# Performance work log

Hardware: AMD Instinct MI355X
Metric: run time of the kernel (lower is better)

Reference implementation:

```python
import jax, jax.numpy as jnp
import numpy as np

SEGMENT_LENGTHS = [1024, 2048, 4096]
DILATION_RATES = [1, 2, 4]


def _head_groups(num_heads, num_segments):
    base = num_heads // num_segments
    extra = num_heads % num_segments
    groups = [base] * num_segments
    for i in range(extra):
        groups[-(i + 1)] += 1
    return groups


def _dilated_indices(segment_len, dilation_rate, offset):
    # Mirrors RingDilatedAttentionV2._apply_dilation index construction (static).
    if dilation_rate > 1:
        idx = np.arange(offset, segment_len, dilation_rate)
        repeats = (segment_len + len(idx) - 1) // len(idx)
        idx = np.tile(idx, repeats)[:segment_len] % segment_len
    else:
        idx = np.arange(segment_len)
    return jnp.asarray(idx, dtype=jnp.int32)


def setup_inputs() -> dict:
    key = jax.random.key(0)
    kq, kk, kv = jax.random.split(key, 3)
    b, n, h, d = 1, 4096, 12, 64
    return {
        "query": jax.random.normal(kq, (b, n, h, d), dtype=jnp.float32),
        "key": jax.random.normal(kk, (b, n, h, d), dtype=jnp.float32),
        "value": jax.random.normal(kv, (b, n, h, d), dtype=jnp.float32),
        "is_causal": 1,
    }


def _dilated_attention(query, key, value, is_causal):
    b, n, h, d = query.shape
    groups = _head_groups(h, len(SEGMENT_LENGTHS))
    scale = 1.0 / np.sqrt(d).astype(np.float32)
    outs = []
    head_start = 0
    for i, (seg_len, rate, g) in enumerate(zip(SEGMENT_LENGTHS, DILATION_RATES, groups)):
        if g == 0:
            continue
        sl = min(seg_len, n)
        ns = n // sl  # n chosen divisible by every segment length
        q = query[:, :, head_start:head_start + g, :].reshape(b, ns, sl, g, d)
        k = key[:, :, head_start:head_start + g, :].reshape(b, ns, sl, g, d)
        v = value[:, :, head_start:head_start + g, :].reshape(b, ns, sl, g, d)
        if rate > 1 or i > 0:
            idx = _dilated_indices(sl, rate, i)
            k = k[:, :, idx]
            v = v[:, :, idx]
        # scores: [b, seg, heads, q_pos, k_pos]
        scores = jnp.einsum("bsqhd,bskhd->bshqk", q, k) * scale
        if is_causal:
            causal = jnp.triu(jnp.ones((sl, sl), dtype=bool), k=1)
            scores = jnp.where(causal, jnp.finfo(scores.dtype).min, scores)
        attn = jax.nn.softmax(scores, axis=-1)
        o = jnp.einsum("bshqk,bskhd->bsqhd", attn, v).reshape(b, n, g, d)
        outs.append(o)
        head_start += g
    return jnp.concatenate(outs, axis=2)  # [b, n, h, d]


def reference(query, key, value, is_causal):
    return _dilated_attention(query, key, value, is_causal)
```

## Files before the change

kernel.cpp:

```cpp
#include <hip/hip_runtime.h>
#include <hip/hip_bf16.h>
#include <math.h>

typedef __bf16 bf16x8 __attribute__((ext_vector_type(8)));
typedef float  f32x4  __attribute__((ext_vector_type(4)));
typedef float  f32x16 __attribute__((ext_vector_type(16)));
typedef int    int2v  __attribute__((ext_vector_type(2)));
typedef unsigned int uint4v __attribute__((ext_vector_type(4)));
typedef unsigned short ushort_t;

#define LDK 72

#define KG_OFF  0
#define VGT_OFF 6291456
#define LACC_OFF 12582912
#define CTR_OFF  12779520

struct ItemTab { unsigned short v[896]; int n; };

constexpr ItemTab build_items(int causal) {
    ItemTab t{};
    for (int i = 0; i < 896; ++i) t.v[i] = 0xFFFF;
    t.n = 0;
    for (int cost = 16; cost >= 1; --cost)
        for (int qt = 31; qt >= 0; --qt)
            for (int h = 11; h >= 0; --h) {
                const int group = h >> 2;
                const int sl = 1024 << group;
                const int qb = (qt << 7) & (sl - 1);
                const int nkt = causal ? (((qb + 127) >> 6) + 1) : (sl >> 6);
                for (int c = 0; c < 4; ++c) {
                    const int kt0 = c << 4;
                    if (kt0 >= nkt) continue;
                    const int rem = nkt - kt0;
                    const int cst = rem < 16 ? rem : 16;
                    if (cst == cost) t.v[t.n++] = (unsigned short)((qt << 6) | (h << 2) | c);
                }
            }
    return t;
}

__constant__ ItemTab g_tab_c = build_items(1);
__constant__ ItemTab g_tab_n = build_items(0);

__device__ __forceinline__ int gather_pos(int gi, int group) {
    const int lsl = 10 + group;
    const int seg = gi >> lsl;
    const int j   = gi - (seg << lsl);
    return (seg << lsl) + group + ((j & 1023) << group);
}

__device__ __forceinline__ void gld_lds16(const ushort_t* g, __bf16* l) {
    __builtin_amdgcn_global_load_lds(
        (const __attribute__((address_space(1))) void*)g,
        (__attribute__((address_space(3))) void*)l, 16, 0, 0);
}

__device__ __forceinline__ unsigned int pk_bf16(float lo, float hi) {
    unsigned short a = __builtin_bit_cast(unsigned short, (__bf16)lo);
    unsigned short b = __builtin_bit_cast(unsigned short, (__bf16)hi);
    return ((unsigned int)b << 16) | (unsigned int)a;
}

__device__ __forceinline__ f32x16 zero16() {
    f32x16 z;
    #pragma unroll
    for (int i = 0; i < 16; ++i) z[i] = 0.f;
    return z;
}

__global__ __launch_bounds__(256)
void preconvert_kernel(const float* __restrict__ K, const float* __restrict__ V,
                       ushort_t* __restrict__ Kg, ushort_t* __restrict__ VgT,
                       float* __restrict__ Out, float* __restrict__ l_acc,
                       int* __restrict__ ctr)
{
    const int HD = 768;
    int b = blockIdx.x;
    const int tid = threadIdx.x;
    if (b < 768) {
        if (b == 0 && tid == 0) *ctr = 0;
        {
            float4 z = {0.f, 0.f, 0.f, 0.f};
            float4* zp = (float4*)Out + ((size_t)b * 256 + tid) * 4;
            zp[0] = z; zp[1] = z; zp[2] = z; zp[3] = z;
        }
        const int h = b % 12, gi0 = (b / 12) * 64;
        const int group = h >> 2;
        const int gi = gi0 + (tid >> 2);
        const int d0 = (tid & 3) << 4;
        const int pos = gather_pos(gi, group);
        const float* kp = K + (size_t)pos * HD + h * 64 + d0;
        float4 x0 = ((const float4*)kp)[0], x1 = ((const float4*)kp)[1];
        float4 x2 = ((const float4*)kp)[2], x3 = ((const float4*)kp)[3];
        bf16x8 w0, w1;
        w0[0]=(__bf16)x0.x; w0[1]=(__bf16)x0.y; w0[2]=(__bf16)x0.z; w0[3]=(__bf16)x0.w;
        w0[4]=(__bf16)x1.x; w0[5]=(__bf16)x1.y; w0[6]=(__bf16)x1.z; w0[7]=(__bf16)x1.w;
        w1[0]=(__bf16)x2.x; w1[1]=(__bf16)x2.y; w1[2]=(__bf16)x2.z; w1[3]=(__bf16)x2.w;
        w1[4]=(__bf16)x3.x; w1[5]=(__bf16)x3.y; w1[6]=(__bf16)x3.z; w1[7]=(__bf16)x3.w;
        ushort_t* out = Kg + ((size_t)(h * 4096 + gi)) * 64 + d0;
        *(bf16x8*)out = w0;
        *(bf16x8*)(out + 8) = w1;
    } else {
        b -= 768;
        if (b < 192) l_acc[b * 256 + tid] = 0.f;
        const int h = b % 12, gi0 = (b / 12) * 64;
        const int group = h >> 2;
        __shared__ __align__(16) __bf16 Ts[64 * LDK];
        const int gil = tid >> 2;
        const int d0 = (tid & 3) << 4;
        const int pos = gather_pos(gi0 + gil, group);
        const float* vp = V + (size_t)pos * HD + h * 64 + d0;
        float4 x0 = ((const float4*)vp)[0], x1 = ((const float4*)vp)[1];
        float4 x2 = ((const float4*)vp)[2], x3 = ((const float4*)vp)[3];
        bf16x8 w0, w1;
        w0[0]=(__bf16)x0.x; w0[1]=(__bf16)x0.y; w0[2]=(__bf16)x0.z; w0[3]=(__bf16)x0.w;
        w0[4]=(__bf16)x1.x; w0[5]=(__bf16)x1.y; w0[6]=(__bf16)x1.z; w0[7]=(__bf16)x1.w;
        w1[0]=(__bf16)x2.x; w1[1]=(__bf16)x2.y; w1[2]=(__bf16)x2.z; w1[3]=(__bf16)x2.w;
        w1[4]=(__bf16)x3.x; w1[5]=(__bf16)x3.y; w1[6]=(__bf16)x3.z; w1[7]=(__bf16)x3.w;
        *(bf16x8*)&Ts[gil * LDK + d0]     = w0;
        *(bf16x8*)&Ts[gil * LDK + d0 + 8] = w1;
        __syncthreads();
        const int d = tid >> 2, c = tid & 3;
        bf16x8 o0, o1;
        #pragma unroll
        for (int i = 0; i < 8; ++i) {
            o0[i] = Ts[(c * 16 + i) * LDK + d];
            o1[i] = Ts[(c * 16 + 8 + i) * LDK + d];
        }
        ushort_t* out = VgT + ((size_t)(h * 64 + d)) * 4096 + gi0 + c * 16;
        *(bf16x8*)out = o0;
        *(bf16x8*)(out + 8) = o1;
    }
}

__global__ __launch_bounds__(256)
void dilated_attn_kernel(const float* __restrict__ Q,
                         const ushort_t* __restrict__ Kg,
                         const ushort_t* __restrict__ VgT,
                         const int* __restrict__ is_causal_p,
                         float* __restrict__ Out,
                         float* __restrict__ l_acc,
                         int* __restrict__ ctr)
{
    const int HD = 768;
    const int causal = (*is_causal_p) != 0;
    const ItemTab& tab = causal ? g_tab_c : g_tab_n;
    const int n_items = tab.n;

    const int tid  = threadIdx.x;
    const int wave = tid >> 6;
    const int lane = tid & 63;
    const int l31  = lane & 31;
    const int hi   = lane >> 5;

    __shared__ __align__(16) __bf16 Ks[2][64 * 64];
    __shared__ __align__(16) __bf16 Vs[2][64 * 64];
    __shared__ int s_item;

    const int bx16 = (((lane & 7) ^ (lane >> 3)) & 7) << 3;
    const int r8   = lane >> 3;

    for (;;) {
        if (tid == 0) s_item = atomicAdd(ctr, 1);
        __syncthreads();
        const int n = s_item;
        __syncthreads();
        if (n >= n_items) break;

        const int enc = tab.v[n];
        const int qt  = enc >> 6;
        const int h   = (enc >> 2) & 15;
        const int c   = enc & 3;
        const int group = h >> 2;
        const int sl    = 1024 << group;

        const int q0 = qt << 7;
        const int qb = q0 & (sl - 1);
        const int seg_start = q0 - qb;
        const int blk_diag = (qb + 127) >> 6;
        const int nkt = causal ? (blk_diag + 1) : (sl >> 6);
        const int kt0 = c << 4;
        const int kend = min(kt0 + 16, nkt);
        const int nch  = (nkt + 15) >> 4;

        const ushort_t* kg_head = Kg + (size_t)h * 4096 * 64;
        const ushort_t* vt_head = VgT + (size_t)h * 64 * 4096;

        auto stage = [&](int kt, int buf) {
            const ushort_t* kb = kg_head + ((size_t)(seg_start + (kt << 6)) << 6);
            const ushort_t* vb = vt_head + seg_start + (kt << 6);
            #pragma unroll
            for (int i = 0; i < 2; ++i) {
                const int row = i * 32 + wave * 8 + r8;
                gld_lds16(kb + row * 64 + bx16, &Ks[buf][(i * 32 + wave * 8) * 64]);
                gld_lds16(vb + (size_t)row * 4096 + bx16, &Vs[buf][(i * 32 + wave * 8) * 64]);
            }
        };

        stage(kt0, 0);

        const int qrow = q0 + wave * 32 + l31;
        const float* qptr = Q + (size_t)qrow * HD + h * 64;
        bf16x8 qf[4];
        {
            const float s = 0.125f * 1.4426950408889634f;
            #pragma unroll
            for (int ds = 0; ds < 4; ++ds) {
                float4 x0 = ((const float4*)(qptr + ds * 16 + hi * 8))[0];
                float4 x1 = ((const float4*)(qptr + ds * 16 + hi * 8))[1];
                bf16x8 w;
                w[0]=(__bf16)(x0.x*s); w[1]=(__bf16)(x0.y*s); w[2]=(__bf16)(x0.z*s); w[3]=(__bf16)(x0.w*s);
                w[4]=(__bf16)(x1.x*s); w[5]=(__bf16)(x1.y*s); w[6]=(__bf16)(x1.z*s); w[7]=(__bf16)(x1.w*s);
                qf[ds] = w;
            }
        }

        const int mydiag = causal ? ((qb + wave * 32 + 31) >> 6) : 0x7fffffff;
        const int lrow   = ((wave & 1) << 5) + l31;

        f32x16 o0 = zero16(), o1 = zero16();
        float l_part = 0.f;

        for (int kt = kt0; kt < kend; ++kt) {
            const int cur = (kt - kt0) & 1;

            asm volatile("s_waitcnt vmcnt(0)" ::: "memory");
            __builtin_amdgcn_s_barrier();
            __builtin_amdgcn_sched_barrier(0);

            if (kt + 1 < kend) stage(kt + 1, cur ^ 1);

            if (kt <= mydiag) {
                f32x16 s0 = zero16(), s1 = zero16();
                const int xr = (l31 & 7);
                __builtin_amdgcn_s_setprio(1);
                #pragma unroll
                for (int ds = 0; ds < 4; ++ds) {
                    const int cb = ds * 2 + hi;
                    bf16x8 k0 = *(const bf16x8*)&Ks[cur][l31 * 64        + ((cb ^ xr) << 3)];
                    bf16x8 k1 = *(const bf16x8*)&Ks[cur][(32 + l31) * 64 + ((cb ^ xr) << 3)];
                    s0 = __builtin_amdgcn_mfma_f32_32x32x16_bf16(k0, qf[ds], s0, 0, 0, 0);
                    s1 = __builtin_amdgcn_mfma_f32_32x32x16_bf16(k1, qf[ds], s1, 0, 0, 0);
                }
                __builtin_amdgcn_s_setprio(0);

                float p[2][16];
                const bool isdiag = causal && (kt == mydiag);
                #pragma unroll
                for (int r = 0; r < 16; ++r) {
                    float v0 = __builtin_amdgcn_exp2f(s0[r]);
                    float v1 = __builtin_amdgcn_exp2f(s1[r]);
                    if (isdiag) {
                        const int kl = (r & 3) + ((r >> 2) << 3) + (hi << 2);
                        if (kl > lrow)      v0 = 0.f;
                        if (kl + 32 > lrow) v1 = 0.f;
                    }
                    p[0][r] = v0; p[1][r] = v1;
                    l_part += v0 + v1;
                }

                __builtin_amdgcn_s_setprio(1);
                #pragma unroll
                for (int b = 0; b < 2; ++b) {
                    #pragma unroll
                    for (int ks2 = 0; ks2 < 2; ++ks2) {
                        const int g = ks2 * 8;
                        int x0 = (int)pk_bf16(p[b][g + 0], p[b][g + 1]);
                        int x1 = (int)pk_bf16(p[b][g + 2], p[b][g + 3]);
                        int y0 = (int)pk_bf16(p[b][g + 4], p[b][g + 5]);
                        int y1 = (int)pk_bf16(p[b][g + 6], p[b][g + 7]);
                        int2v r02 = __builtin_amdgcn_permlane32_swap(x0, y0, false, false);
                        int2v r13 = __builtin_amdgcn_permlane32_swap(x1, y1, false, false);
                        uint4v t;
                        t[0] = (unsigned int)r02[0];
                        t[1] = (unsigned int)r13[0];
                        t[2] = (unsigned int)r02[1];
                        t[3] = (unsigned int)r13[1];
                        bf16x8 pa = __builtin_bit_cast(bf16x8, t);
                        const int kcb = (b * 2 + ks2) * 2 + hi;
                        bf16x8 v0 = *(const bf16x8*)&Vs[cur][l31 * 64        + ((kcb ^ xr) << 3)];
                        bf16x8 v1 = *(const bf16x8*)&Vs[cur][(32 + l31) * 64 + ((kcb ^ xr) << 3)];
                        o0 = __builtin_amdgcn_mfma_f32_32x32x16_bf16(pa, v0, o0, 0, 0, 0);
                        o1 = __builtin_amdgcn_mfma_f32_32x32x16_bf16(pa, v1, o1, 0, 0, 0);
                    }
                }
                __builtin_amdgcn_s_setprio(0);
            }
        }

        const float l2 = l_part + __shfl_xor(l_part, 32);
        const int qw = q0 + wave * 32;
        if (nch == 1) {
            const float inv = 1.0f / l2;
            #pragma unroll
            for (int r = 0; r < 16; ++r) {
                const int qloc = (r & 3) + ((r >> 2) << 3) + (hi << 2);
                const float invq = __shfl(inv, qloc);
                const int row = qw + qloc;
                Out[(size_t)row * HD + h * 64 + l31]      = o0[r] * invq;
                Out[(size_t)row * HD + h * 64 + 32 + l31] = o1[r] * invq;
            }
        } else {
            if (hi == 0) atomicAdd(&l_acc[(qw + l31) * 12 + h], l2);
            #pragma unroll
            for (int r = 0; r < 16; ++r) {
                const int qloc = (r & 3) + ((r >> 2) << 3) + (hi << 2);
                const int row = qw + qloc;
                atomicAdd(&Out[(size_t)row * HD + h * 64 + l31],      o0[r]);
                atomicAdd(&Out[(size_t)row * HD + h * 64 + 32 + l31], o1[r]);
            }
        }
    }
}

__global__ __launch_bounds__(256)
void finalize_kernel(float* __restrict__ Out, const float* __restrict__ l_acc,
                     const int* __restrict__ is_causal_p)
{
    const int causal = (*is_causal_p) != 0;
    const int idx = blockIdx.x * 256 + threadIdx.x;
    const int rh = idx >> 4;
    const int d4 = idx & 15;
    const int h = rh % 12;
    const int row = rh / 12;
    const int group = h >> 2;
    const int ntf = 16 << group;
    const int qt128 = row >> 7;
    const int qb_t = (qt128 << 1) & (ntf - 1);
    const int nkt = causal ? (qb_t + 2) : ntf;
    if (nkt <= 16) return;
    const float inv = 1.0f / l_acc[rh];
    float4* p = (float4*)Out + (size_t)rh * 16 + d4;
    float4 v = *p;
    v.x *= inv; v.y *= inv; v.z *= inv; v.w *= inv;
    *p = v;
}

extern "C" void kernel_launch(void* const* d_in, const int* in_sizes, int n_in,
                              void* d_out, int out_size, void* d_ws, size_t ws_size,
                              hipStream_t stream) {
    (void)in_sizes; (void)n_in; (void)out_size; (void)ws_size;
    const float* Q = (const float*)d_in[0];
    const float* K = (const float*)d_in[1];
    const float* V = (const float*)d_in[2];
    const int* isc = (const int*)d_in[3];
    float* Out = (float*)d_out;
    ushort_t* Kg   = (ushort_t*)((char*)d_ws + KG_OFF);
    ushort_t* VgT  = (ushort_t*)((char*)d_ws + VGT_OFF);
    float*    lacc = (float*)((char*)d_ws + LACC_OFF);
    int*      ctr  = (int*)((char*)d_ws + CTR_OFF);

    preconvert_kernel<<<1536, 256, 0, stream>>>(K, V, Kg, VgT, Out, lacc, ctr);
    dilated_attn_kernel<<<512, 256, 0, stream>>>(Q, Kg, VgT, isc, Out, lacc, ctr);
    finalize_kernel<<<3072, 256, 0, stream>>>(Out, lacc, isc);
}
```

Measured before the change: 135.2 us.

## Fuse preconvert, attention and finalize into one cooperative kernel with grid syncs

Merges the three launches into a single cooperative kernel of 512 blocks that runs grid-stride preconvert units, then the attention work queue, then finalize, separated by grid.sync. Preconvert K is rewritten to read each source row once and write it to all its dilated gather slots. Zeroing of Out is limited to rows that take multi-chunk atomics. The aim is to remove launch gaps and redundant global traffic, at the cost of grid-wide barriers and higher LDS use per block, which could cut occupancy. A fallback to the three-kernel path is kept in case the cooperative launch fails.

```diff
diff --git a/kernel.cpp b/kernel.cpp
--- a/kernel.cpp
+++ b/kernel.cpp
@@ -1,6 +1,9 @@
 #include <hip/hip_runtime.h>
 #include <hip/hip_bf16.h>
+#include <hip/hip_cooperative_groups.h>
 #include <math.h>
+
+namespace cg = cooperative_groups;
 
 typedef __bf16 bf16x8 __attribute__((ext_vector_type(8)));
 typedef float  f32x4  __attribute__((ext_vector_type(4)));
@@ -69,44 +72,60 @@
     return z;
 }
 
-__global__ __launch_bounds__(256)
-void preconvert_kernel(const float* __restrict__ K, const float* __restrict__ V,
-                       ushort_t* __restrict__ Kg, ushort_t* __restrict__ VgT,
-                       float* __restrict__ Out, float* __restrict__ l_acc,
-                       int* __restrict__ ctr)
+__device__ __forceinline__ void preconvert_unit(
+    int b, int tid, const float* __restrict__ K, const float* __restrict__ V,
+    ushort_t* __restrict__ Kg, ushort_t* __restrict__ VgT,
+    float* __restrict__ Out, float* __restrict__ l_acc,
+    int* __restrict__ ctr, int causal, __bf16* Ts)
 {
     const int HD = 768;
-    int b = blockIdx.x;
-    const int tid = threadIdx.x;
     if (b < 768) {
         if (b == 0 && tid == 0) *ctr = 0;
         {
-            float4 z = {0.f, 0.f, 0.f, 0.f};
-            float4* zp = (float4*)Out + ((size_t)b * 256 + tid) * 4;
-            zp[0] = z; zp[1] = z; zp[2] = z; zp[3] = z;
-        }
-        const int h = b % 12, gi0 = (b / 12) * 64;
+            const int rh = (b * 256 + tid) >> 2;
+            const int h_ = rh % 12;
+            const int row_ = rh / 12;
+            const int ntf = 16 << (h_ >> 2);
+            const int qt128 = row_ >> 7;
+            const int qb_t = (qt128 << 1) & (ntf - 1);
+            const int nkt = causal ? (qb_t + 2) : ntf;
+            if (nkt > 16) {
+                float4 z = {0.f, 0.f, 0.f, 0.f};
+                float4* zp = (float4*)Out + ((size_t)b * 256 + tid) * 4;
+                zp[0] = z; zp[1] = z; zp[2] = z; zp[3] = z;
+            }
+        }
+        const int h = b % 12, p0 = (b / 12) * 64;
         const int group = h >> 2;
-        const int gi = gi0 + (tid >> 2);
+        const int pos = p0 + (tid >> 2);
         const int d0 = (tid & 3) << 4;
-        const int pos = gather_pos(gi, group);
-        const float* kp = K + (size_t)pos * HD + h * 64 + d0;
-        float4 x0 = ((const float4*)kp)[0], x1 = ((const float4*)kp)[1];
-        float4 x2 = ((const float4*)kp)[2], x3 = ((const float4*)kp)[3];
-        bf16x8 w0, w1;
-        w0[0]=(__bf16)x0.x; w0[1]=(__bf16)x0.y; w0[2]=(__bf16)x0.z; w0[3]=(__bf16)x0.w;
-        w0[4]=(__bf16)x1.x; w0[5]=(__bf16)x1.y; w0[6]=(__bf16)x1.z; w0[7]=(__bf16)x1.w;
-        w1[0]=(__bf16)x2.x; w1[1]=(__bf16)x2.y; w1[2]=(__bf16)x2.z; w1[3]=(__bf16)x2.w;
-        w1[4]=(__bf16)x3.x; w1[5]=(__bf16)x3.y; w1[6]=(__bf16)x3.z; w1[7]=(__bf16)x3.w;
-        ushort_t* out = Kg + ((size_t)(h * 4096 + gi)) * 64 + d0;
-        *(bf16x8*)out = w0;
-        *(bf16x8*)(out + 8) = w1;
+        const int lsl = 10 + group;
+        const int rate = 1 << group;
+        const int seg_base = (pos >> lsl) << lsl;
+        const int po = pos - seg_base;
+        const int rem = po - group;
+        if (rem >= 0 && (rem & (rate - 1)) == 0) {
+            const float* kp = K + (size_t)pos * HD + h * 64 + d0;
+            float4 x0 = ((const float4*)kp)[0], x1 = ((const float4*)kp)[1];
+            float4 x2 = ((const float4*)kp)[2], x3 = ((const float4*)kp)[3];
+            bf16x8 w0, w1;
+            w0[0]=(__bf16)x0.x; w0[1]=(__bf16)x0.y; w0[2]=(__bf16)x0.z; w0[3]=(__bf16)x0.w;
+            w0[4]=(__bf16)x1.x; w0[5]=(__bf16)x1.y; w0[6]=(__bf16)x1.z; w0[7]=(__bf16)x1.w;
+            w1[0]=(__bf16)x2.x; w1[1]=(__bf16)x2.y; w1[2]=(__bf16)x2.z; w1[3]=(__bf16)x2.w;
+            w1[4]=(__bf16)x3.x; w1[5]=(__bf16)x3.y; w1[6]=(__bf16)x3.z; w1[7]=(__bf16)x3.w;
+            const int jb = rem >> group;
+            for (int k = 0; k < rate; ++k) {
+                const int gi = seg_base + jb + (k << 10);
+                ushort_t* out = Kg + ((size_t)(h * 4096 + gi)) * 64 + d0;
+                *(bf16x8*)out = w0;
+                *(bf16x8*)(out + 8) = w1;
+            }
+        }
     } else {
         b -= 768;
         if (b < 192) l_acc[b * 256 + tid] = 0.f;
         const int h = b % 12, gi0 = (b / 12) * 64;
         const int group = h >> 2;
-        __shared__ __align__(16) __bf16 Ts[64 * LDK];
         const int gil = tid >> 2;
         const int d0 = (tid & 3) << 4;
         const int pos = gather_pos(gi0 + gil, group);
@@ -131,20 +150,17 @@
         ushort_t* out = VgT + ((size_t)(h * 64 + d)) * 4096 + gi0 + c * 16;
         *(bf16x8*)out = o0;
         *(bf16x8*)(out + 8) = o1;
+        __syncthreads();
     }
 }
 
-__global__ __launch_bounds__(256)
-void dilated_attn_kernel(const float* __restrict__ Q,
-                         const ushort_t* __restrict__ Kg,
-                         const ushort_t* __restrict__ VgT,
-                         const int* __restrict__ is_causal_p,
-                         float* __restrict__ Out,
-                         float* __restrict__ l_acc,
-                         int* __restrict__ ctr)
+__device__ __forceinline__ void attn_phase(
+    const float* __restrict__ Q, const ushort_t* __restrict__ Kg,
+    const ushort_t* __restrict__ VgT, int causal,
+    float* __restrict__ Out, float* __restrict__ l_acc, int* __restrict__ ctr,
+    __bf16 (*Ks)[64 * 64], __bf16 (*Vs)[64 * 64], int* s_item)
 {
     const int HD = 768;
-    const int causal = (*is_causal_p) != 0;
     const ItemTab& tab = causal ? g_tab_c : g_tab_n;
     const int n_items = tab.n;
 
@@ -154,17 +170,13 @@
     const int l31  = lane & 31;
     const int hi   = lane >> 5;
 
-    __shared__ __align__(16) __bf16 Ks[2][64 * 64];
-    __shared__ __align__(16) __bf16 Vs[2][64 * 64];
-    __shared__ int s_item;
-
     const int bx16 = (((lane & 7) ^ (lane >> 3)) & 7) << 3;
     const int r8   = lane >> 3;
 
     for (;;) {
-        if (tid == 0) s_item = atomicAdd(ctr, 1);
+        if (tid == 0) *s_item = atomicAdd(ctr, 1);
         __syncthreads();
-        const int n = s_item;
+        const int n = *s_item;
         __syncthreads();
         if (n >= n_items) break;
 
@@ -261,6 +273,7 @@
                 }
 
                 __builtin_amdgcn_s_setprio(1);
+                const int xr2 = (l31 & 7);
                 #pragma unroll
                 for (int b = 0; b < 2; ++b) {
                     #pragma unroll
@@ -279,8 +292,8 @@
                         t[3] = (unsigned int)r13[1];
                         bf16x8 pa = __builtin_bit_cast(bf16x8, t);
                         const int kcb = (b * 2 + ks2) * 2 + hi;
-                        bf16x8 v0 = *(const bf16x8*)&Vs[cur][l31 * 64        + ((kcb ^ xr) << 3)];
-                        bf16x8 v1 = *(const bf16x8*)&Vs[cur][(32 + l31) * 64 + ((kcb ^ xr) << 3)];
+                        bf16x8 v0 = *(const bf16x8*)&Vs[cur][l31 * 64        + ((kcb ^ xr2) << 3)];
+                        bf16x8 v1 = *(const bf16x8*)&Vs[cur][(32 + l31) * 64 + ((kcb ^ xr2) << 3)];
                         o0 = __builtin_amdgcn_mfma_f32_32x32x16_bf16(pa, v0, o0, 0, 0, 0);
                         o1 = __builtin_amdgcn_mfma_f32_32x32x16_bf16(pa, v1, o1, 0, 0, 0);
                     }
@@ -314,18 +327,14 @@
     }
 }
 
-__global__ __launch_bounds__(256)
-void finalize_kernel(float* __restrict__ Out, const float* __restrict__ l_acc,
-                     const int* __restrict__ is_causal_p)
-{
-    const int causal = (*is_causal_p) != 0;
-    const int idx = blockIdx.x * 256 + threadIdx.x;
+__device__ __forceinline__ void finalize_unit(
+    int idx, float* __restrict__ Out, const float* __restrict__ l_acc, int causal)
+{
     const int rh = idx >> 4;
     const int d4 = idx & 15;
     const int h = rh % 12;
     const int row = rh / 12;
-    const int group = h >> 2;
-    const int ntf = 16 << group;
+    const int ntf = 16 << (h >> 2);
     const int qt128 = row >> 7;
     const int qb_t = (qt128 << 1) & (ntf - 1);
     const int nkt = causal ? (qb_t + 2) : ntf;
@@ -335,6 +344,68 @@
     float4 v = *p;
     v.x *= inv; v.y *= inv; v.z *= inv; v.w *= inv;
     *p = v;
+}
+
+__global__ __launch_bounds__(256)
+void fused_kernel(const float* __restrict__ Q, const float* __restrict__ K,
+                  const float* __restrict__ V, const int* __restrict__ is_causal_p,
+                  float* __restrict__ Out, ushort_t* __restrict__ Kg,
+                  ushort_t* __restrict__ VgT, float* __restrict__ l_acc,
+                  int* __restrict__ ctr)
+{
+    __shared__ __align__(16) __bf16 Ks[2][64 * 64];
+    __shared__ __align__(16) __bf16 Vs[2][64 * 64];
+    __shared__ __align__(16) __bf16 Ts[64 * LDK];
+    __shared__ int s_item;
+
+    cg::grid_group grid = cg::this_grid();
+    const int causal = (*is_causal_p) != 0;
+    const int tid = threadIdx.x;
+
+    for (int u = blockIdx.x; u < 1536; u += 512)
+        preconvert_unit(u, tid, K, V, Kg, VgT, Out, l_acc, ctr, causal, Ts);
+
+    grid.sync();
+
+    attn_phase(Q, Kg, VgT, causal, Out, l_acc, ctr, Ks, Vs, &s_item);
+
+    grid.sync();
+
+    for (int base = blockIdx.x; base < 3072; base += 512)
+        finalize_unit(base * 256 + tid, Out, l_acc, causal);
+}
+
+__global__ __launch_bounds__(256)
+void preconvert_kernel(const float* __restrict__ K, const float* __restrict__ V,
+                       ushort_t* __restrict__ Kg, ushort_t* __restrict__ VgT,
+                       float* __restrict__ Out, float* __restrict__ l_acc,
+                       int* __restrict__ ctr, const int* __restrict__ is_causal_p)
+{
+    __shared__ __align__(16) __bf16 Ts[64 * LDK];
+    preconvert_unit(blockIdx.x, threadIdx.x, K, V, Kg, VgT, Out, l_acc, ctr,
+                    (*is_causal_p) != 0, Ts);
+}
+
+__global__ __launch_bounds__(256)
+void dilated_attn_kernel(const float* __restrict__ Q,
+                         const ushort_t* __restrict__ Kg,
+                         const ushort_t* __restrict__ VgT,
+                         const int* __restrict__ is_causal_p,
+                         float* __restrict__ Out,
+                         float* __restrict__ l_acc,
+                         int* __restrict__ ctr)
+{
+    __shared__ __align__(16) __bf16 Ks[2][64 * 64];
+    __shared__ __align__(16) __bf16 Vs[2][64 * 64];
+    __shared__ int s_item;
+    attn_phase(Q, Kg, VgT, (*is_causal_p) != 0, Out, l_acc, ctr, Ks, Vs, &s_item);
+}
+
+__global__ __launch_bounds__(256)
+void finalize_kernel(float* __restrict__ Out, const float* __restrict__ l_acc,
+                     const int* __restrict__ is_causal_p)
+{
+    finalize_unit(blockIdx.x * 256 + threadIdx.x, Out, l_acc, (*is_causal_p) != 0);
 }
 
 extern "C" void kernel_launch(void* const* d_in, const int* in_sizes, int n_in,
@@ -351,7 +422,14 @@
     float*    lacc = (float*)((char*)d_ws + LACC_OFF);
     int*      ctr  = (int*)((char*)d_ws + CTR_OFF);
 
-    preconvert_kernel<<<1536, 256, 0, stream>>>(K, V, Kg, VgT, Out, lacc, ctr);
-    dilated_attn_kernel<<<512, 256, 0, stream>>>(Q, Kg, VgT, isc, Out, lacc, ctr);
-    finalize_kernel<<<3072, 256, 0, stream>>>(Out, lacc, isc);
-}
+    void* args[] = {(void*)&Q, (void*)&K, (void*)&V, (void*)&isc, (void*)&Out,
+                    (void*)&Kg, (void*)&VgT, (void*)&lacc, (void*)&ctr};
+    hipError_t e = hipLaunchCooperativeKernel((const void*)fused_kernel,
+                                              dim3(512), dim3(256), args, 0, stream);
+    if (e != hipSuccess) {
+        (void)hipGetLastError();
+        preconvert_kernel<<<1536, 256, 0, stream>>>(K, V, Kg, VgT, Out, lacc, ctr, isc);
+        dilated_attn_kernel<<<512, 256, 0, stream>>>(Q, Kg, VgT, isc, Out, lacc, ctr);
+        finalize_kernel<<<3072, 256, 0, stream>>>(Out, lacc, isc);
+    }
+}
```

New measurement: 275.7 us. +103.9%, slower.

## Halve split-K chunk size, double persistent grid, dedupe K gather writes

Applied to the files above, without the earlier changes.

Work items now cover 8 key tiles instead of 16, which doubles the item count and gives finer load balancing. The persistent grid grows to 1024 blocks with a launch bound of 4 waves per SIMD. The K preconversion reads each source row once and writes it to every replicated gather slot. The output zeroing is skipped for rows that a single chunk writes directly. More items produce more atomic partial-sum adds into the output, and the V LDS swizzle index changes to use l31&7.

```diff
diff --git a/kernel.cpp b/kernel.cpp
--- a/kernel.cpp
+++ b/kernel.cpp
@@ -16,25 +16,25 @@
 #define LACC_OFF 12582912
 #define CTR_OFF  12779520
 
-struct ItemTab { unsigned short v[896]; int n; };
+struct ItemTab { unsigned short v[1792]; int n; };
 
 constexpr ItemTab build_items(int causal) {
     ItemTab t{};
-    for (int i = 0; i < 896; ++i) t.v[i] = 0xFFFF;
+    for (int i = 0; i < 1792; ++i) t.v[i] = 0xFFFF;
     t.n = 0;
-    for (int cost = 16; cost >= 1; --cost)
+    for (int cost = 8; cost >= 1; --cost)
         for (int qt = 31; qt >= 0; --qt)
             for (int h = 11; h >= 0; --h) {
                 const int group = h >> 2;
                 const int sl = 1024 << group;
                 const int qb = (qt << 7) & (sl - 1);
                 const int nkt = causal ? (((qb + 127) >> 6) + 1) : (sl >> 6);
-                for (int c = 0; c < 4; ++c) {
-                    const int kt0 = c << 4;
+                for (int c = 0; c < 8; ++c) {
+                    const int kt0 = c << 3;
                     if (kt0 >= nkt) continue;
                     const int rem = nkt - kt0;
-                    const int cst = rem < 16 ? rem : 16;
-                    if (cst == cost) t.v[t.n++] = (unsigned short)((qt << 6) | (h << 2) | c);
+                    const int cst = rem < 8 ? rem : 8;
+                    if (cst == cost) t.v[t.n++] = (unsigned short)((qt << 7) | (h << 3) | c);
                 }
             }
     return t;
@@ -73,7 +73,7 @@
 void preconvert_kernel(const float* __restrict__ K, const float* __restrict__ V,
                        ushort_t* __restrict__ Kg, ushort_t* __restrict__ VgT,
                        float* __restrict__ Out, float* __restrict__ l_acc,
-                       int* __restrict__ ctr)
+                       int* __restrict__ ctr, const int* __restrict__ is_causal_p)
 {
     const int HD = 768;
     int b = blockIdx.x;
@@ -81,26 +81,46 @@
     if (b < 768) {
         if (b == 0 && tid == 0) *ctr = 0;
         {
-            float4 z = {0.f, 0.f, 0.f, 0.f};
-            float4* zp = (float4*)Out + ((size_t)b * 256 + tid) * 4;
-            zp[0] = z; zp[1] = z; zp[2] = z; zp[3] = z;
-        }
-        const int h = b % 12, gi0 = (b / 12) * 64;
+            const int causal = (*is_causal_p) != 0;
+            const int rh = (b * 256 + tid) >> 2;
+            const int h_ = rh % 12;
+            const int row_ = rh / 12;
+            const int ntf = 16 << (h_ >> 2);
+            const int qt128 = row_ >> 7;
+            const int qb_t = (qt128 << 1) & (ntf - 1);
+            const int nkt = causal ? (qb_t + 2) : ntf;
+            if (nkt > 8) {
+                float4 z = {0.f, 0.f, 0.f, 0.f};
+                float4* zp = (float4*)Out + ((size_t)b * 256 + tid) * 4;
+                zp[0] = z; zp[1] = z; zp[2] = z; zp[3] = z;
+            }
+        }
+        const int h = b % 12, p0 = (b / 12) * 64;
         const int group = h >> 2;
-        const int gi = gi0 + (tid >> 2);
+        const int pos = p0 + (tid >> 2);
         const int d0 = (tid & 3) << 4;
-        const int pos = gather_pos(gi, group);
-        const float* kp = K + (size_t)pos * HD + h * 64 + d0;
-        float4 x0 = ((const float4*)kp)[0], x1 = ((const float4*)kp)[1];
-        float4 x2 = ((const float4*)kp)[2], x3 = ((const float4*)kp)[3];
-        bf16x8 w0, w1;
-        w0[0]=(__bf16)x0.x; w0[1]=(__bf16)x0.y; w0[2]=(__bf16)x0.z; w0[3]=(__bf16)x0.w;
-        w0[4]=(__bf16)x1.x; w0[5]=(__bf16)x1.y; w0[6]=(__bf16)x1.z; w0[7]=(__bf16)x1.w;
-        w1[0]=(__bf16)x2.x; w1[1]=(__bf16)x2.y; w1[2]=(__bf16)x2.z; w1[3]=(__bf16)x2.w;
-        w1[4]=(__bf16)x3.x; w1[5]=(__bf16)x3.y; w1[6]=(__bf16)x3.z; w1[7]=(__bf16)x3.w;
-        ushort_t* out = Kg + ((size_t)(h * 4096 + gi)) * 64 + d0;
-        *(bf16x8*)out = w0;
-        *(bf16x8*)(out + 8) = w1;
+        const int lsl = 10 + group;
+        const int rate = 1 << group;
+        const int seg_base = (pos >> lsl) << lsl;
+        const int po = pos - seg_base;
+        const int rem = po - group;
+        if (rem >= 0 && (rem & (rate - 1)) == 0) {
+            const float* kp = K + (size_t)pos * HD + h * 64 + d0;
+            float4 x0 = ((const float4*)kp)[0], x1 = ((const float4*)kp)[1];
+            float4 x2 = ((const float4*)kp)[2], x3 = ((const float4*)kp)[3];
+            bf16x8 w0, w1;
+            w0[0]=(__bf16)x0.x; w0[1]=(__bf16)x0.y; w0[2]=(__bf16)x0.z; w0[3]=(__bf16)x0.w;
+            w0[4]=(__bf16)x1.x; w0[5]=(__bf16)x1.y; w0[6]=(__bf16)x1.z; w0[7]=(__bf16)x1.w;
+            w1[0]=(__bf16)x2.x; w1[1]=(__bf16)x2.y; w1[2]=(__bf16)x2.z; w1[3]=(__bf16)x2.w;
+            w1[4]=(__bf16)x3.x; w1[5]=(__bf16)x3.y; w1[6]=(__bf16)x3.z; w1[7]=(__bf16)x3.w;
+            const int jb = rem >> group;
+            for (int k = 0; k < rate; ++k) {
+                const int gi = seg_base + jb + (k << 10);
+                ushort_t* out = Kg + ((size_t)(h * 4096 + gi)) * 64 + d0;
+                *(bf16x8*)out = w0;
+                *(bf16x8*)(out + 8) = w1;
+            }
+        }
     } else {
         b -= 768;
         if (b < 192) l_acc[b * 256 + tid] = 0.f;
@@ -134,7 +154,7 @@
     }
 }
 
-__global__ __launch_bounds__(256)
+__global__ __launch_bounds__(256, 4)
 void dilated_attn_kernel(const float* __restrict__ Q,
                          const ushort_t* __restrict__ Kg,
                          const ushort_t* __restrict__ VgT,
@@ -169,9 +189,9 @@
         if (n >= n_items) break;
 
         const int enc = tab.v[n];
-        const int qt  = enc >> 6;
-        const int h   = (enc >> 2) & 15;
-        const int c   = enc & 3;
+        const int qt  = enc >> 7;
+        const int h   = (enc >> 3) & 15;
+        const int c   = enc & 7;
         const int group = h >> 2;
         const int sl    = 1024 << group;
 
@@ -180,9 +200,9 @@
         const int seg_start = q0 - qb;
         const int blk_diag = (qb + 127) >> 6;
         const int nkt = causal ? (blk_diag + 1) : (sl >> 6);
-        const int kt0 = c << 4;
-        const int kend = min(kt0 + 16, nkt);
-        const int nch  = (nkt + 15) >> 4;
+        const int kt0 = c << 3;
+        const int kend = min(kt0 + 8, nkt);
+        const int nch  = (nkt + 7) >> 3;
 
         const ushort_t* kg_head = Kg + (size_t)h * 4096 * 64;
         const ushort_t* vt_head = VgT + (size_t)h * 64 * 4096;
@@ -261,6 +281,7 @@
                 }
 
                 __builtin_amdgcn_s_setprio(1);
+                const int xr2 = (l31 & 7);
                 #pragma unroll
                 for (int b = 0; b < 2; ++b) {
                     #pragma unroll
@@ -279,8 +300,8 @@
                         t[3] = (unsigned int)r13[1];
                         bf16x8 pa = __builtin_bit_cast(bf16x8, t);
                         const int kcb = (b * 2 + ks2) * 2 + hi;
-                        bf16x8 v0 = *(const bf16x8*)&Vs[cur][l31 * 64        + ((kcb ^ xr) << 3)];
-                        bf16x8 v1 = *(const bf16x8*)&Vs[cur][(32 + l31) * 64 + ((kcb ^ xr) << 3)];
+                        bf16x8 v0 = *(const bf16x8*)&Vs[cur][l31 * 64        + ((kcb ^ xr2) << 3)];
+                        bf16x8 v1 = *(const bf16x8*)&Vs[cur][(32 + l31) * 64 + ((kcb ^ xr2) << 3)];
                         o0 = __builtin_amdgcn_mfma_f32_32x32x16_bf16(pa, v0, o0, 0, 0, 0);
                         o1 = __builtin_amdgcn_mfma_f32_32x32x16_bf16(pa, v1, o1, 0, 0, 0);
                     }
@@ -324,12 +345,11 @@
     const int d4 = idx & 15;
     const int h = rh % 12;
     const int row = rh / 12;
-    const int group = h >> 2;
-    const int ntf = 16 << group;
+    const int ntf = 16 << (h >> 2);
     const int qt128 = row >> 7;
     const int qb_t = (qt128 << 1) & (ntf - 1);
     const int nkt = causal ? (qb_t + 2) : ntf;
-    if (nkt <= 16) return;
+    if (nkt <= 8) return;
     const float inv = 1.0f / l_acc[rh];
     float4* p = (float4*)Out + (size_t)rh * 16 + d4;
     float4 v = *p;
@@ -351,7 +371,7 @@
     float*    lacc = (float*)((char*)d_ws + LACC_OFF);
     int*      ctr  = (int*)((char*)d_ws + CTR_OFF);
 
-    preconvert_kernel<<<1536, 256, 0, stream>>>(K, V, Kg, VgT, Out, lacc, ctr);
-    dilated_attn_kernel<<<512, 256, 0, stream>>>(Q, Kg, VgT, isc, Out, lacc, ctr);
+    preconvert_kernel<<<1536, 256, 0, stream>>>(K, V, Kg, VgT, Out, lacc, ctr, isc);
+    dilated_attn_kernel<<<1024, 256, 0, stream>>>(Q, Kg, VgT, isc, Out, lacc, ctr);
     finalize_kernel<<<3072, 256, 0, stream>>>(Out, lacc, isc);
 }
```

Result: slower. 150.6 us (+11.4%).

## Partition attention work into per-XCD bins with XCC-local queues and dedupe K gather

Applied to the files above, without the earlier changes.

Splits the global work-item queue into 8 bins keyed by head, one atomic counter per bin. Each workgroup reads its XCC id and drains its own bin first, then moves round-robin to the others, so K/V tiles for a head tend to stay in one XCD's L2. The K preconvert now reads each source row once and writes it to every duplicated gather slot instead of gathering per output. Output zeroing is limited to rows that use atomic accumulation. The risks are load imbalance between bins, dependence on the XCC id register, and the added per-row predicate checks.

```diff
diff --git a/kernel.cpp b/kernel.cpp
--- a/kernel.cpp
+++ b/kernel.cpp
@@ -16,27 +16,33 @@
 #define LACC_OFF 12582912
 #define CTR_OFF  12779520
 
-struct ItemTab { unsigned short v[896]; int n; };
+struct ItemTab { unsigned short v[896]; int beg[9]; };
 
 constexpr ItemTab build_items(int causal) {
     ItemTab t{};
     for (int i = 0; i < 896; ++i) t.v[i] = 0xFFFF;
-    t.n = 0;
-    for (int cost = 16; cost >= 1; --cost)
-        for (int qt = 31; qt >= 0; --qt)
-            for (int h = 11; h >= 0; --h) {
-                const int group = h >> 2;
-                const int sl = 1024 << group;
-                const int qb = (qt << 7) & (sl - 1);
-                const int nkt = causal ? (((qb + 127) >> 6) + 1) : (sl >> 6);
-                for (int c = 0; c < 4; ++c) {
-                    const int kt0 = c << 4;
-                    if (kt0 >= nkt) continue;
-                    const int rem = nkt - kt0;
-                    const int cst = rem < 16 ? rem : 16;
-                    if (cst == cost) t.v[t.n++] = (unsigned short)((qt << 6) | (h << 2) | c);
-                }
-            }
+    const int head2bin[12] = {4, 5, 6, 7, 4, 5, 6, 7, 0, 1, 2, 3};
+    int n = 0;
+    for (int bin = 0; bin < 8; ++bin) {
+        t.beg[bin] = n;
+        for (int cost = 16; cost >= 1; --cost)
+            for (int qt = 31; qt >= 0; --qt)
+                for (int h = 11; h >= 0; --h) {
+                    if (head2bin[h] != bin) continue;
+                    const int group = h >> 2;
+                    const int sl = 1024 << group;
+                    const int qb = (qt << 7) & (sl - 1);
+                    const int nkt = causal ? (((qb + 127) >> 6) + 1) : (sl >> 6);
+                    for (int c = 0; c < 4; ++c) {
+                        const int kt0 = c << 4;
+                        if (kt0 >= nkt) continue;
+                        const int rem = nkt - kt0;
+                        const int cst = rem < 16 ? rem : 16;
+                        if (cst == cost) t.v[n++] = (unsigned short)((qt << 6) | (h << 2) | c);
+                    }
+                }
+    }
+    t.beg[8] = n;
     return t;
 }
 
@@ -73,34 +79,54 @@
 void preconvert_kernel(const float* __restrict__ K, const float* __restrict__ V,
                        ushort_t* __restrict__ Kg, ushort_t* __restrict__ VgT,
                        float* __restrict__ Out, float* __restrict__ l_acc,
-                       int* __restrict__ ctr)
+                       int* __restrict__ ctr, const int* __restrict__ is_causal_p)
 {
     const int HD = 768;
     int b = blockIdx.x;
     const int tid = threadIdx.x;
     if (b < 768) {
-        if (b == 0 && tid == 0) *ctr = 0;
+        if (b == 0 && tid < 8) ctr[tid] = 0;
         {
-            float4 z = {0.f, 0.f, 0.f, 0.f};
-            float4* zp = (float4*)Out + ((size_t)b * 256 + tid) * 4;
-            zp[0] = z; zp[1] = z; zp[2] = z; zp[3] = z;
+            const int causal = (*is_causal_p) != 0;
+            const int rh = (b * 256 + tid) >> 2;
+            const int h_ = rh % 12;
+            const int row_ = rh / 12;
+            const int ntf = 16 << (h_ >> 2);
+            const int qt128 = row_ >> 7;
+            const int qb_t = (qt128 << 1) & (ntf - 1);
+            const int nkt = causal ? (qb_t + 2) : ntf;
+            if (nkt > 16) {
+                float4 z = {0.f, 0.f, 0.f, 0.f};
+                float4* zp = (float4*)Out + ((size_t)b * 256 + tid) * 4;
+                zp[0] = z; zp[1] = z; zp[2] = z; zp[3] = z;
+            }
         }
-        const int h = b % 12, gi0 = (b / 12) * 64;
+        const int h = b % 12, p0 = (b / 12) * 64;
         const int group = h >> 2;
-        const int gi = gi0 + (tid >> 2);
+        const int pos = p0 + (tid >> 2);
         const int d0 = (tid & 3) << 4;
-        const int pos = gather_pos(gi, group);
-        const float* kp = K + (size_t)pos * HD + h * 64 + d0;
-        float4 x0 = ((const float4*)kp)[0], x1 = ((const float4*)kp)[1];
-        float4 x2 = ((const float4*)kp)[2], x3 = ((const float4*)kp)[3];
-        bf16x8 w0, w1;
-        w0[0]=(__bf16)x0.x; w0[1]=(__bf16)x0.y; w0[2]=(__bf16)x0.z; w0[3]=(__bf16)x0.w;
-        w0[4]=(__bf16)x1.x; w0[5]=(__bf16)x1.y; w0[6]=(__bf16)x1.z; w0[7]=(__bf16)x1.w;
-        w1[0]=(__bf16)x2.x; w1[1]=(__bf16)x2.y; w1[2]=(__bf16)x2.z; w1[3]=(__bf16)x2.w;
-        w1[4]=(__bf16)x3.x; w1[5]=(__bf16)x3.y; w1[6]=(__bf16)x3.z; w1[7]=(__bf16)x3.w;
-        ushort_t* out = Kg + ((size_t)(h * 4096 + gi)) * 64 + d0;
-        *(bf16x8*)out = w0;
-        *(bf16x8*)(out + 8) = w1;
+        const int lsl = 10 + group;
+        const int rate = 1 << group;
+        const int seg_base = (pos >> lsl) << lsl;
+        const int po = pos - seg_base;
+        const int rem = po - group;
+        if (rem >= 0 && (rem & (rate - 1)) == 0) {
+            const float* kp = K + (size_t)pos * HD + h * 64 + d0;
+            float4 x0 = ((const float4*)kp)[0], x1 = ((const float4*)kp)[1];
+            float4 x2 = ((const float4*)kp)[2], x3 = ((const float4*)kp)[3];
+            bf16x8 w0, w1;
+            w0[0]=(__bf16)x0.x; w0[1]=(__bf16)x0.y; w0[2]=(__bf16)x0.z; w0[3]=(__bf16)x0.w;
+            w0[4]=(__bf16)x1.x; w0[5]=(__bf16)x1.y; w0[6]=(__bf16)x1.z; w0[7]=(__bf16)x1.w;
+            w1[0]=(__bf16)x2.x; w1[1]=(__bf16)x2.y; w1[2]=(__bf16)x2.z; w1[3]=(__bf16)x2.w;
+            w1[4]=(__bf16)x3.x; w1[5]=(__bf16)x3.y; w1[6]=(__bf16)x3.z; w1[7]=(__bf16)x3.w;
+            const int jb = rem >> group;
+            for (int k = 0; k < rate; ++k) {
+                const int gi = seg_base + jb + (k << 10);
+                ushort_t* out = Kg + ((size_t)(h * 4096 + gi)) * 64 + d0;
+                *(bf16x8*)out = w0;
+                *(bf16x8*)(out + 8) = w1;
+            }
+        }
     } else {
         b -= 768;
         if (b < 192) l_acc[b * 256 + tid] = 0.f;
@@ -146,7 +172,6 @@
     const int HD = 768;
     const int causal = (*is_causal_p) != 0;
     const ItemTab& tab = causal ? g_tab_c : g_tab_n;
-    const int n_items = tab.n;
 
     const int tid  = threadIdx.x;
     const int wave = tid >> 6;
@@ -158,157 +183,165 @@
     __shared__ __align__(16) __bf16 Vs[2][64 * 64];
     __shared__ int s_item;
 
+    unsigned int xcc = 0;
+    asm volatile("s_getreg_b32 %0, hwreg(HW_REG_XCC_ID)" : "=s"(xcc));
+    const int myx = (int)(xcc & 7);
+
     const int bx16 = (((lane & 7) ^ (lane >> 3)) & 7) << 3;
     const int r8   = lane >> 3;
 
-    for (;;) {
-        if (tid == 0) s_item = atomicAdd(ctr, 1);
-        __syncthreads();
-        const int n = s_item;
-        __syncthreads();
-        if (n >= n_items) break;
-
-        const int enc = tab.v[n];
-        const int qt  = enc >> 6;
-        const int h   = (enc >> 2) & 15;
-        const int c   = enc & 3;
-        const int group = h >> 2;
-        const int sl    = 1024 << group;
-
-        const int q0 = qt << 7;
-        const int qb = q0 & (sl - 1);
-        const int seg_start = q0 - qb;
-        const int blk_diag = (qb + 127) >> 6;
-        const int nkt = causal ? (blk_diag + 1) : (sl >> 6);
-        const int kt0 = c << 4;
-        const int kend = min(kt0 + 16, nkt);
-        const int nch  = (nkt + 15) >> 4;
-
-        const ushort_t* kg_head = Kg + (size_t)h * 4096 * 64;
-        const ushort_t* vt_head = VgT + (size_t)h * 64 * 4096;
-
-        auto stage = [&](int kt, int buf) {
-            const ushort_t* kb = kg_head + ((size_t)(seg_start + (kt << 6)) << 6);
-            const ushort_t* vb = vt_head + seg_start + (kt << 6);
-            #pragma unroll
-            for (int i = 0; i < 2; ++i) {
-                const int row = i * 32 + wave * 8 + r8;
-                gld_lds16(kb + row * 64 + bx16, &Ks[buf][(i * 32 + wave * 8) * 64]);
-                gld_lds16(vb + (size_t)row * 4096 + bx16, &Vs[buf][(i * 32 + wave * 8) * 64]);
-            }
-        };
-
-        stage(kt0, 0);
-
-        const int qrow = q0 + wave * 32 + l31;
-        const float* qptr = Q + (size_t)qrow * HD + h * 64;
-        bf16x8 qf[4];
-        {
-            const float s = 0.125f * 1.4426950408889634f;
-            #pragma unroll
-            for (int ds = 0; ds < 4; ++ds) {
-                float4 x0 = ((const float4*)(qptr + ds * 16 + hi * 8))[0];
-                float4 x1 = ((const float4*)(qptr + ds * 16 + hi * 8))[1];
-                bf16x8 w;
-                w[0]=(__bf16)(x0.x*s); w[1]=(__bf16)(x0.y*s); w[2]=(__bf16)(x0.z*s); w[3]=(__bf16)(x0.w*s);
-                w[4]=(__bf16)(x1.x*s); w[5]=(__bf16)(x1.y*s); w[6]=(__bf16)(x1.z*s); w[7]=(__bf16)(x1.w*s);
-                qf[ds] = w;
-            }
-        }
-
-        const int mydiag = causal ? ((qb + wave * 32 + 31) >> 6) : 0x7fffffff;
-        const int lrow   = ((wave & 1) << 5) + l31;
-
-        f32x16 o0 = zero16(), o1 = zero16();
-        float l_part = 0.f;
-
-        for (int kt = kt0; kt < kend; ++kt) {
-            const int cur = (kt - kt0) & 1;
-
-            asm volatile("s_waitcnt vmcnt(0)" ::: "memory");
-            __builtin_amdgcn_s_barrier();
-            __builtin_amdgcn_sched_barrier(0);
-
-            if (kt + 1 < kend) stage(kt + 1, cur ^ 1);
-
-            if (kt <= mydiag) {
-                f32x16 s0 = zero16(), s1 = zero16();
-                const int xr = (l31 & 7);
-                __builtin_amdgcn_s_setprio(1);
+    for (int ring = 0; ring < 8; ++ring) {
+        const int bin = (myx + ring) & 7;
+        const int lo = tab.beg[bin], hicap = tab.beg[bin + 1];
+        for (;;) {
+            if (tid == 0) s_item = lo + atomicAdd(&ctr[bin], 1);
+            __syncthreads();
+            const int n = s_item;
+            __syncthreads();
+            if (n >= hicap) break;
+
+            const int enc = tab.v[n];
+            const int qt  = enc >> 6;
+            const int h   = (enc >> 2) & 15;
+            const int c   = enc & 3;
+            const int group = h >> 2;
+            const int sl    = 1024 << group;
+
+            const int q0 = qt << 7;
+            const int qb = q0 & (sl - 1);
+            const int seg_start = q0 - qb;
+            const int blk_diag = (qb + 127) >> 6;
+            const int nkt = causal ? (blk_diag + 1) : (sl >> 6);
+            const int kt0 = c << 4;
+            const int kend = min(kt0 + 16, nkt);
+            const int nch  = (nkt + 15) >> 4;
+
+            const ushort_t* kg_head = Kg + (size_t)h * 4096 * 64;
+            const ushort_t* vt_head = VgT + (size_t)h * 64 * 4096;
+
+            auto stage = [&](int kt, int buf) {
+                const ushort_t* kb = kg_head + ((size_t)(seg_start + (kt << 6)) << 6);
+                const ushort_t* vb = vt_head + seg_start + (kt << 6);
+                #pragma unroll
+                for (int i = 0; i < 2; ++i) {
+                    const int row = i * 32 + wave * 8 + r8;
+                    gld_lds16(kb + row * 64 + bx16, &Ks[buf][(i * 32 + wave * 8) * 64]);
+                    gld_lds16(vb + (size_t)row * 4096 + bx16, &Vs[buf][(i * 32 + wave * 8) * 64]);
+                }
+            };
+
+            stage(kt0, 0);
+
+            const int qrow = q0 + wave * 32 + l31;
+            const float* qptr = Q + (size_t)qrow * HD + h * 64;
+            bf16x8 qf[4];
+            {
+                const float s = 0.125f * 1.4426950408889634f;
                 #pragma unroll
                 for (int ds = 0; ds < 4; ++ds) {
-                    const int cb = ds * 2 + hi;
-                    bf16x8 k0 = *(const bf16x8*)&Ks[cur][l31 * 64        + ((cb ^ xr) << 3)];
-                    bf16x8 k1 = *(const bf16x8*)&Ks[cur][(32 + l31) * 64 + ((cb ^ xr) << 3)];
-                    s0 = __builtin_amdgcn_mfma_f32_32x32x16_bf16(k0, qf[ds], s0, 0, 0, 0);
-                    s1 = __builtin_amdgcn_mfma_f32_32x32x16_bf16(k1, qf[ds], s1, 0, 0, 0);
-                }
-                __builtin_amdgcn_s_setprio(0);
-
-                float p[2][16];
-                const bool isdiag = causal && (kt == mydiag);
+                    float4 x0 = ((const float4*)(qptr + ds * 16 + hi * 8))[0];
+                    float4 x1 = ((const float4*)(qptr + ds * 16 + hi * 8))[1];
+                    bf16x8 w;
+                    w[0]=(__bf16)(x0.x*s); w[1]=(__bf16)(x0.y*s); w[2]=(__bf16)(x0.z*s); w[3]=(__bf16)(x0.w*s);
+                    w[4]=(__bf16)(x1.x*s); w[5]=(__bf16)(x1.y*s); w[6]=(__bf16)(x1.z*s); w[7]=(__bf16)(x1.w*s);
+                    qf[ds] = w;
+                }
+            }
+
+            const int mydiag = causal ? ((qb + wave * 32 + 31) >> 6) : 0x7fffffff;
+            const int lrow   = ((wave & 1) << 5) + l31;
+
+            f32x16 o0 = zero16(), o1 = zero16();
+            float l_part = 0.f;
+
+            for (int kt = kt0; kt < kend; ++kt) {
+                const int cur = (kt - kt0) & 1;
+
+                asm volatile("s_waitcnt vmcnt(0)" ::: "memory");
+                __builtin_amdgcn_s_barrier();
+                __builtin_amdgcn_sched_barrier(0);
+
+                if (kt + 1 < kend) stage(kt + 1, cur ^ 1);
+
+                if (kt <= mydiag) {
+                    f32x16 s0 = zero16(), s1 = zero16();
+                    const int xr = (l31 & 7);
+                    __builtin_amdgcn_s_setprio(1);
+                    #pragma unroll
+                    for (int ds = 0; ds < 4; ++ds) {
+                        const int cb = ds * 2 + hi;
+                        bf16x8 k0 = *(const bf16x8*)&Ks[cur][l31 * 64        + ((cb ^ xr) << 3)];
+                        bf16x8 k1 = *(const bf16x8*)&Ks[cur][(32 + l31) * 64 + ((cb ^ xr) << 3)];
+                        s0 = __builtin_amdgcn_mfma_f32_32x32x16_bf16(k0, qf[ds], s0, 0, 0, 0);
+                        s1 = __builtin_amdgcn_mfma_f32_32x32x16_bf16(k1, qf[ds], s1, 0, 0, 0);
+                    }
+                    __builtin_amdgcn_s_setprio(0);
+
+                    float p[2][16];
+                    const bool isdiag = causal && (kt == mydiag);
+                    #pragma unroll
+                    for (int r = 0; r < 16; ++r) {
+                        float v0 = __builtin_amdgcn_exp2f(s0[r]);
+                        float v1 = __builtin_amdgcn_exp2f(s1[r]);
+                        if (isdiag) {
+                            const int kl = (r & 3) + ((r >> 2) << 3) + (hi << 2);
+                            if (kl > lrow)      v0 = 0.f;
+                            if (kl + 32 > lrow) v1 = 0.f;
+                        }
+                        p[0][r] = v0; p[1][r] = v1;
+                        l_part += v0 + v1;
+                    }
+
+                    __builtin_amdgcn_s_setprio(1);
+                    #pragma unroll
+                    for (int b = 0; b < 2; ++b) {
+                        #pragma unroll
+                        for (int ks2 = 0; ks2 < 2; ++ks2) {
+                            const int g = ks2 * 8;
+                            int x0 = (int)pk_bf16(p[b][g + 0], p[b][g + 1]);
+                            int x1 = (int)pk_bf16(p[b][g + 2], p[b][g + 3]);
+                            int y0 = (int)pk_bf16(p[b][g + 4], p[b][g + 5]);
+                            int y1 = (int)pk_bf16(p[b][g + 6], p[b][g + 7]);
+                            int2v r02 = __builtin_amdgcn_permlane32_swap(x0, y0, false, false);
+                            int2v r13 = __builtin_amdgcn_permlane32_swap(x1, y1, false, false);
+                            uint4v t;
+                            t[0] = (unsigned int)r02[0];
+                            t[1] = (unsigned int)r13[0];
+                            t[2] = (unsigned int)r02[1];
+                            t[3] = (unsigned int)r13[1];
+                            bf16x8 pa = __builtin_bit_cast(bf16x8, t);
+                            const int kcb = (b * 2 + ks2) * 2 + hi;
+                            bf16x8 v0 = *(const bf16x8*)&Vs[cur][l31 * 64        + ((kcb ^ xr) << 3)];
+                            bf16x8 v1 = *(const bf16x8*)&Vs[cur][(32 + l31) * 64 + ((kcb ^ xr) << 3)];
+                            o0 = __builtin_amdgcn_mfma_f32_32x32x16_bf16(pa, v0, o0, 0, 0, 0);
+                            o1 = __builtin_amdgcn_mfma_f32_32x32x16_bf16(pa, v1, o1, 0, 0, 0);
+                        }
+                    }
+                    __builtin_amdgcn_s_setprio(0);
+                }
+            }
+
+            const float l2 = l_part + __shfl_xor(l_part, 32);
+            const int qw = q0 + wave * 32;
+            if (nch == 1) {
+                const float inv = 1.0f / l2;
                 #pragma unroll
                 for (int r = 0; r < 16; ++r) {
-                    float v0 = __builtin_amdgcn_exp2f(s0[r]);
-                    float v1 = __builtin_amdgcn_exp2f(s1[r]);
-                    if (isdiag) {
-                        const int kl = (r & 3) + ((r >> 2) << 3) + (hi << 2);
-                        if (kl > lrow)      v0 = 0.f;
-                        if (kl + 32 > lrow) v1 = 0.f;
-                    }
-                    p[0][r] = v0; p[1][r] = v1;
-                    l_part += v0 + v1;
-                }
-
-                __builtin_amdgcn_s_setprio(1);
+                    const int qloc = (r & 3) + ((r >> 2) << 3) + (hi << 2);
+                    const float invq = __shfl(inv, qloc);
+                    const int row = qw + qloc;
+                    Out[(size_t)row * HD + h * 64 + l31]      = o0[r] * invq;
+                    Out[(size_t)row * HD + h * 64 + 32 + l31] = o1[r] * invq;
+                }
+            } else {
+                if (hi == 0) atomicAdd(&l_acc[(qw + l31) * 12 + h], l2);
                 #pragma unroll
-                for (int b = 0; b < 2; ++b) {
-                    #pragma unroll
-                    for (int ks2 = 0; ks2 < 2; ++ks2) {
-                        const int g = ks2 * 8;
-                        int x0 = (int)pk_bf16(p[b][g + 0], p[b][g + 1]);
-                        int x1 = (int)pk_bf16(p[b][g + 2], p[b][g + 3]);
-                        int y0 = (int)pk_bf16(p[b][g + 4], p[b][g + 5]);
-                        int y1 = (int)pk_bf16(p[b][g + 6], p[b][g + 7]);
-                        int2v r02 = __builtin_amdgcn_permlane32_swap(x0, y0, false, false);
-                        int2v r13 = __builtin_amdgcn_permlane32_swap(x1, y1, false, false);
-                        uint4v t;
-                        t[0] = (unsigned int)r02[0];
-                        t[1] = (unsigned int)r13[0];
-                        t[2] = (unsigned int)r02[1];
-                        t[3] = (unsigned int)r13[1];
-                        bf16x8 pa = __builtin_bit_cast(bf16x8, t);
-                        const int kcb = (b * 2 + ks2) * 2 + hi;
-                        bf16x8 v0 = *(const bf16x8*)&Vs[cur][l31 * 64        + ((kcb ^ xr) << 3)];
-                        bf16x8 v1 = *(const bf16x8*)&Vs[cur][(32 + l31) * 64 + ((kcb ^ xr) << 3)];
-                        o0 = __builtin_amdgcn_mfma_f32_32x32x16_bf16(pa, v0, o0, 0, 0, 0);
-                        o1 = __builtin_amdgcn_mfma_f32_32x32x16_bf16(pa, v1, o1, 0, 0, 0);
-                    }
-                }
-                __builtin_amdgcn_s_setprio(0);
-            }
-        }
-
-        const float l2 = l_part + __shfl_xor(l_part, 32);
-        const int qw = q0 + wave * 32;
-        if (nch == 1) {
-            const float inv = 1.0f / l2;
-            #pragma unroll
-            for (int r = 0; r < 16; ++r) {
-                const int qloc = (r & 3) + ((r >> 2) << 3) + (hi << 2);
-                const float invq = __shfl(inv, qloc);
-                const int row = qw + qloc;
-                Out[(size_t)row * HD + h * 64 + l31]      = o0[r] * invq;
-                Out[(size_t)row * HD + h * 64 + 32 + l31] = o1[r] * invq;
-            }
-        } else {
-            if (hi == 0) atomicAdd(&l_acc[(qw + l31) * 12 + h], l2);
-            #pragma unroll
-            for (int r = 0; r < 16; ++r) {
-                const int qloc = (r & 3) + ((r >> 2) << 3) + (hi << 2);
-                const int row = qw + qloc;
-                atomicAdd(&Out[(size_t)row * HD + h * 64 + l31],      o0[r]);
-                atomicAdd(&Out[(size_t)row * HD + h * 64 + 32 + l31], o1[r]);
+                for (int r = 0; r < 16; ++r) {
+                    const int qloc = (r & 3) + ((r >> 2) << 3) + (hi << 2);
+                    const int row = qw + qloc;
+                    atomicAdd(&Out[(size_t)row * HD + h * 64 + l31],      o0[r]);
+                    atomicAdd(&Out[(size_t)row * HD + h * 64 + 32 + l31], o1[r]);
+                }
             }
         }
     }
@@ -324,8 +357,7 @@
     const int d4 = idx & 15;
     const int h = rh % 12;
     const int row = rh / 12;
-    const int group = h >> 2;
-    const int ntf = 16 << group;
+    const int ntf = 16 << (h >> 2);
     const int qt128 = row >> 7;
     const int qb_t = (qt128 << 1) & (ntf - 1);
     const int nkt = causal ? (qb_t + 2) : ntf;
@@ -351,7 +383,7 @@
     float*    lacc = (float*)((char*)d_ws + LACC_OFF);
     int*      ctr  = (int*)((char*)d_ws + CTR_OFF);
 
-    preconvert_kernel<<<1536, 256, 0, stream>>>(K, V, Kg, VgT, Out, lacc, ctr);
+    preconvert_kernel<<<1536, 256, 0, stream>>>(K, V, Kg, VgT, Out, lacc, ctr, isc);
     dilated_attn_kernel<<<512, 256, 0, stream>>>(Q, Kg, VgT, isc, Out, lacc, ctr);
     finalize_kernel<<<3072, 256, 0, stream>>>(Out, lacc, isc);
 }
```

Result: slower. 164.1 us (+21.4%).
